# Kernel tuning notes

Hardware: AMD Instinct MI355X
Metric: run time of the kernel (lower is better)

Reference implementation:

```python
import jax, jax.numpy as jnp
import numpy as np

EMBED_DIM = 1024
B, C, H, W = 32, 1024, 32, 32


def _conv1x1(x, w, b):
    # x: [B,C,H,W], w: [O,C] (squeezed 1x1 conv kernel), b: [O]
    return jnp.einsum('bchw,oc->bohw', x, w) + b[None, :, None, None]


def setup_inputs() -> dict:
    key = jax.random.key(0)
    ks = jax.random.split(key, 12)
    s = 1.0 / np.sqrt(C)  # torch Conv2d default init scale (uniform bound)
    inp = {
        'shape_map': jax.random.normal(ks[0], (B, C, H, W), jnp.float32),
        'img_map': jax.random.normal(ks[1], (B, C, H, W), jnp.float32),
        'wq': jax.random.uniform(ks[2], (C, C), jnp.float32, -s, s),
        'bq': jax.random.uniform(ks[3], (C,), jnp.float32, -s, s),
        'wk': jax.random.uniform(ks[4], (C, C), jnp.float32, -s, s),
        'bk': jax.random.uniform(ks[5], (C,), jnp.float32, -s, s),
        'wv': jax.random.uniform(ks[6], (C, C), jnp.float32, -s, s),
        'bv': jax.random.uniform(ks[7], (C,), jnp.float32, -s, s),
        'wc': jax.random.uniform(ks[8], (C, C), jnp.float32, -s, s),
        'bc': jax.random.uniform(ks[9], (C,), jnp.float32, -s, s),
    }
    return inp


def reference(shape_map, img_map, wq, bq, wk, bk, wv, bv, wc, bc):
    # QKV embeddings: 1x1 conv + tanh (dropout is identity at inference)
    q = jnp.tanh(_conv1x1(shape_map, wq, bq))  # [B,C,H,W]
    k = jnp.tanh(_conv1x1(img_map, wk, bk))
    v = jnp.tanh(_conv1x1(img_map, wv, bv))

    hw = H * W
    q_flat = q.reshape(B, C, hw)
    k_flat = k.reshape(B, C, hw)
    v_flat = v.reshape(B, C, hw)

    # channel-attention: scores over channel pairs, contracted over spatial HW
    scores = jnp.einsum('bcs,bds->bcd', q_flat, k_flat) / jnp.sqrt(
        jnp.asarray(C, q_flat.dtype))  # [B,C,C]
    weights = jax.nn.softmax(scores, axis=-1)
    new_v = jnp.einsum('bcd,bds->bcs', weights, v_flat).reshape(B, C, H, W)

    out = _conv1x1(new_v, wc, bc) + shape_map
    return out
```

## Files before the change

### kernel.cpp

```cpp
#include <hip/hip_runtime.h>


typedef __bf16 bf16x8 __attribute__((ext_vector_type(8)));
typedef float floatx4 __attribute__((ext_vector_type(4)));

__device__ __forceinline__ unsigned short f2bf(float f) {
  union { float f; unsigned int u; } c; c.f = f;
  unsigned int u = c.u;
  u += 0x7fffu + ((u >> 16) & 1u);
  return (unsigned short)(u >> 16);
}

__device__ __forceinline__ float tanh_fast(float x) {
  x = fminf(15.0f, fmaxf(-15.0f, x));
  float t = __expf(2.0f * x);
  return (t - 1.0f) / (t + 1.0f);
}

__device__ __forceinline__ void gemm_core(
    const unsigned short* __restrict__ Ab,
    const unsigned short* __restrict__ Bb,
    int m0, int n0,
    unsigned short* lA, unsigned short* lB,
    floatx4 acc[4][4])
{
  constexpr int K = 1024;
  const int tid  = threadIdx.x;
  const int w    = tid >> 6;
  const int lane = tid & 63;
  const int quad = lane >> 4;
  const int lm   = lane & 15;
  const int wm   = (w >> 1) * 64;
  const int wn   = (w & 1) * 64;
  const int xr   = lm & 7;

  const int srow = lane >> 3;
  const int sg   = (lane & 7) ^ srow;
  const unsigned short* gA0 = Ab + (size_t)(m0 + srow) * K + sg * 8;
  const unsigned short* gB0 = Bb + (size_t)(n0 + srow) * K + sg * 8;

  for (int k0 = 0; k0 < K; k0 += 64) {
#pragma unroll
    for (int i = 0; i < 4; ++i) {
      const int q = w * 4 + i;
      __builtin_amdgcn_global_load_lds(
          (__attribute__((address_space(1))) void*)(gA0 + (size_t)q * 8 * K + k0),
          (__attribute__((address_space(3))) void*)(lA + q * 512), 16, 0, 0);
      __builtin_amdgcn_global_load_lds(
          (__attribute__((address_space(1))) void*)(gB0 + (size_t)q * 8 * K + k0),
          (__attribute__((address_space(3))) void*)(lB + q * 512), 16, 0, 0);
    }
    __syncthreads();

#pragma unroll
    for (int ks = 0; ks < 2; ++ks) {
      bf16x8 af[4], bfv[4];
#pragma unroll
      for (int i = 0; i < 4; ++i) {
        const int row = wm + 16 * i + lm;
        af[i] = *(const bf16x8*)(lA + row * 64 + (((ks * 4 + quad) ^ xr) * 8));
      }
#pragma unroll
      for (int j = 0; j < 4; ++j) {
        const int row = wn + 16 * j + lm;
        bfv[j] = *(const bf16x8*)(lB + row * 64 + (((ks * 4 + quad) ^ xr) * 8));
      }
#pragma unroll
      for (int i = 0; i < 4; ++i)
#pragma unroll
        for (int j = 0; j < 4; ++j)
          acc[i][j] = __builtin_amdgcn_mfma_f32_16x16x32_bf16(
              af[i], bfv[j], acc[i][j], 0, 0, 0);
    }
    __syncthreads();
  }
}

template<int OUT_F32, int BIAS_MODE , int TANH_ON, int RESID_ON>
__global__ __launch_bounds__(256, 2)
void gemm_bt(const unsigned short* __restrict__ A,
             const unsigned short* __restrict__ B,
             void* __restrict__ Cv,
             const float* __restrict__ bias,
             const float* __restrict__ resid,
             float scale,
             size_t sA, size_t sB, size_t sC, size_t sR)
{
  __shared__ unsigned short lA[128 * 64];
  __shared__ unsigned short lB[128 * 64];
  const int m0 = blockIdx.y * 128, n0 = blockIdx.x * 128;
  const int lane = threadIdx.x & 63, w = threadIdx.x >> 6;
  const int quad = lane >> 4, lm = lane & 15;
  const int wm = (w >> 1) * 64, wn = (w & 1) * 64;

  floatx4 acc[4][4];
#pragma unroll
  for (int i = 0; i < 4; ++i)
#pragma unroll
    for (int j = 0; j < 4; ++j) acc[i][j] = (floatx4)(0.0f);

  gemm_core(A + blockIdx.z * sA, B + blockIdx.z * sB, m0, n0, lA, lB, acc);

  float* Cf = (float*)Cv + blockIdx.z * sC;
  unsigned short* Cb = (unsigned short*)Cv + blockIdx.z * sC;
  const float* rp = RESID_ON ? (resid + blockIdx.z * sR) : (const float*)0;

#pragma unroll
  for (int i = 0; i < 4; ++i) {
    const int mbase = m0 + wm + 16 * i + quad * 4;
#pragma unroll
    for (int j = 0; j < 4; ++j) {
      const int n = n0 + wn + 16 * j + lm;
#pragma unroll
      for (int r = 0; r < 4; ++r) {
        const int m = mbase + r;
        float val = acc[i][j][r] * scale;
        if (BIAS_MODE == 1) val += bias[m];
        if (BIAS_MODE == 2) val += bias[n];
        if (TANH_ON) val = tanh_fast(val);
        if (RESID_ON) val += rp[(size_t)m * 1024 + n];
        if (OUT_F32) Cf[(size_t)m * 1024 + n] = val;
        else         Cb[(size_t)m * 1024 + n] = f2bf(val);
      }
    }
  }
}

__global__ __launch_bounds__(256, 2)
void qkv_gemm(const unsigned short* __restrict__ wqb,
              const unsigned short* __restrict__ wkb,
              const unsigned short* __restrict__ wvb,
              const unsigned short* __restrict__ Xt,
              const unsigned short* __restrict__ Yt,
              unsigned short* __restrict__ Qb,
              unsigned short* __restrict__ Kb,
              unsigned short* __restrict__ Vt,
              const float* __restrict__ bq,
              const float* __restrict__ bk,
              const float* __restrict__ bv,
              size_t sBf, int nb)
{
  __shared__ unsigned short lA[128 * 64];
  __shared__ unsigned short lB[128 * 64];
  const int z = blockIdx.z;
  int op, b;
  if (z >= 2 * nb)      { op = 2; b = z - 2 * nb; }
  else if (z >= nb)     { op = 1; b = z - nb; }
  else                  { op = 0; b = z; }

  const unsigned short *A, *B;
  unsigned short* C;
  const float* bias;
  int biasM;
  if (op == 0)      { A = wqb;            B = Xt + b * sBf; C = Qb + b * sBf; bias = bq; biasM = 1; }
  else if (op == 1) { A = wkb;            B = Yt + b * sBf; C = Kb + b * sBf; bias = bk; biasM = 1; }
  else              { A = Yt + b * sBf;   B = wvb;          C = Vt + b * sBf; bias = bv; biasM = 0; }

  const int m0 = blockIdx.y * 128, n0 = blockIdx.x * 128;
  const int lane = threadIdx.x & 63, w = threadIdx.x >> 6;
  const int quad = lane >> 4, lm = lane & 15;
  const int wm = (w >> 1) * 64, wn = (w & 1) * 64;

  floatx4 acc[4][4];
#pragma unroll
  for (int i = 0; i < 4; ++i)
#pragma unroll
    for (int j = 0; j < 4; ++j) acc[i][j] = (floatx4)(0.0f);

  gemm_core(A, B, m0, n0, lA, lB, acc);

#pragma unroll
  for (int i = 0; i < 4; ++i) {
    const int mbase = m0 + wm + 16 * i + quad * 4;
#pragma unroll
    for (int j = 0; j < 4; ++j) {
      const int n = n0 + wn + 16 * j + lm;
      const float bn = biasM ? 0.0f : bias[n];
#pragma unroll
      for (int r = 0; r < 4; ++r) {
        const int m = mbase + r;
        float val = acc[i][j][r] + (biasM ? bias[m] : bn);
        val = tanh_fast(val);
        C[(size_t)m * 1024 + n] = f2bf(val);
      }
    }
  }
}

__global__ __launch_bounds__(256)
void transpose2(const float* __restrict__ in0, const float* __restrict__ in1,
                unsigned short* __restrict__ out0, unsigned short* __restrict__ out1,
                size_t sIn, size_t sOut, int nb)
{
  __shared__ float tile[32][33];
  const int z = blockIdx.z;
  const float* in;
  unsigned short* out;
  if (z < nb) { in = in0 + (size_t)z * sIn;        out = out0 + (size_t)z * sOut; }
  else        { in = in1 + (size_t)(z - nb) * sIn; out = out1 + (size_t)(z - nb) * sOut; }

  const int x  = blockIdx.x * 32 + threadIdx.x;
  const int y0 = blockIdx.y * 32;
#pragma unroll
  for (int k = 0; k < 32; k += 8)
    tile[threadIdx.y + k][threadIdx.x] =
        in[(size_t)(y0 + threadIdx.y + k) * 1024 + x];
  __syncthreads();
  const int xo  = blockIdx.y * 32 + threadIdx.x;
  const int yo0 = blockIdx.x * 32;
#pragma unroll
  for (int k = 0; k < 32; k += 8)
    out[(size_t)(yo0 + threadIdx.y + k) * 1024 + xo] =
        f2bf(tile[threadIdx.x][threadIdx.y + k]);
}

__global__ __launch_bounds__(256)
void softmax_rows(const float* __restrict__ S, unsigned short* __restrict__ W,
                  size_t sS, size_t sW)
{
  const float* s = S + blockIdx.y * sS + (size_t)blockIdx.x * 1024;
  unsigned short* w = W + blockIdx.y * sW + (size_t)blockIdx.x * 1024;
  const int t = threadIdx.x;
  float4 v = ((const float4*)s)[t];
  float mx = fmaxf(fmaxf(v.x, v.y), fmaxf(v.z, v.w));
#pragma unroll
  for (int off = 32; off > 0; off >>= 1)
    mx = fmaxf(mx, __shfl_xor(mx, off));
  __shared__ float redm[4], reds[4];
  const int lane = t & 63, wv = t >> 6;
  if (lane == 0) redm[wv] = mx;
  __syncthreads();
  mx = fmaxf(fmaxf(redm[0], redm[1]), fmaxf(redm[2], redm[3]));
  float e0 = __expf(v.x - mx), e1 = __expf(v.y - mx),
        e2 = __expf(v.z - mx), e3 = __expf(v.w - mx);
  float sum = e0 + e1 + e2 + e3;
#pragma unroll
  for (int off = 32; off > 0; off >>= 1)
    sum += __shfl_xor(sum, off);
  if (lane == 0) reds[wv] = sum;
  __syncthreads();
  sum = reds[0] + reds[1] + reds[2] + reds[3];
  const float inv = 1.0f / sum;
  w[4 * t + 0] = f2bf(e0 * inv);
  w[4 * t + 1] = f2bf(e1 * inv);
  w[4 * t + 2] = f2bf(e2 * inv);
  w[4 * t + 3] = f2bf(e3 * inv);
}

__global__ __launch_bounds__(256)
void cvt_all(const float* __restrict__ s0, const float* __restrict__ s1,
             const float* __restrict__ s2, const float* __restrict__ s3,
             unsigned short* __restrict__ d0, unsigned short* __restrict__ d1,
             unsigned short* __restrict__ d2, unsigned short* __restrict__ d3)
{
  const float* in; unsigned short* out;
  switch (blockIdx.y) {
    case 0: in = s0; out = d0; break;
    case 1: in = s1; out = d1; break;
    case 2: in = s2; out = d2; break;
    default: in = s3; out = d3; break;
  }
  const int i = blockIdx.x * 256 + threadIdx.x;
  float4 v = ((const float4*)in)[i];
  ushort4 o;
  o.x = f2bf(v.x); o.y = f2bf(v.y); o.z = f2bf(v.z); o.w = f2bf(v.w);
  ((ushort4*)out)[i] = o;
}

extern "C" void kernel_launch(void* const* d_in, const int* in_sizes, int n_in,
                              void* d_out, int out_size, void* d_ws, size_t ws_size,
                              hipStream_t stream)
{
  const float* shape_map = (const float*)d_in[0];
  const float* img_map   = (const float*)d_in[1];
  const float* wq = (const float*)d_in[2];
  const float* bq = (const float*)d_in[3];
  const float* wk = (const float*)d_in[4];
  const float* bk = (const float*)d_in[5];
  const float* wv = (const float*)d_in[6];
  const float* bv = (const float*)d_in[7];
  const float* wc = (const float*)d_in[8];
  const float* bc = (const float*)d_in[9];
  float* out = (float*)d_out;

  const size_t ELT = 1024 * 1024;
  const size_t MB  = 1024 * 1024;
  char* ws = (char*)d_ws;

  unsigned short* wq_b = (unsigned short*)(ws + 0 * 2 * MB);
  unsigned short* wk_b = (unsigned short*)(ws + 1 * 2 * MB);
  unsigned short* wv_b = (unsigned short*)(ws + 2 * 2 * MB);
  unsigned short* wc_b = (unsigned short*)(ws + 3 * 2 * MB);
  char* slots = ws + 8 * MB;
  const size_t slotBytes = 10 * MB;
  int nslots = (ws_size > 8 * MB + slotBytes)
                   ? (int)((ws_size - 8 * MB) / slotBytes) : 1;
  if (nslots > 32) nslots = 32;
  if (nslots < 1)  nslots = 1;

  cvt_all<<<dim3(1024, 4), 256, 0, stream>>>(wq, wk, wv, wc,
                                             wq_b, wk_b, wv_b, wc_b);

  const size_t sBf = slotBytes / 2;
  const size_t sF  = slotBytes / 4;

  for (int c0 = 0; c0 < 32; c0 += nslots) {
    const int nb = (32 - c0 < nslots) ? (32 - c0) : nslots;

    unsigned short* Xt  = (unsigned short*)(slots + 0);
    unsigned short* Yt  = (unsigned short*)(slots + 2 * MB);
    float*          Sm  = (float*)(slots + 0);
    unsigned short* Qb  = (unsigned short*)(slots + 4 * MB);
    unsigned short* Kb  = (unsigned short*)(slots + 6 * MB);
    unsigned short* Vt  = (unsigned short*)(slots + 8 * MB);
    unsigned short* Wsm = Qb;
    unsigned short* NVt = Kb;

    transpose2<<<dim3(32, 32, 2 * nb), dim3(32, 8), 0, stream>>>(
        shape_map + (size_t)c0 * ELT, img_map + (size_t)c0 * ELT,
        Xt, Yt, ELT, sBf, nb);

    qkv_gemm<<<dim3(8, 8, 3 * nb), 256, 0, stream>>>(
        wq_b, wk_b, wv_b, Xt, Yt, Qb, Kb, Vt, bq, bk, bv, sBf, nb);

    gemm_bt<1, 0, 0, 0><<<dim3(8, 8, nb), 256, 0, stream>>>(
        Qb, Kb, Sm, nullptr, nullptr, 0.03125f, sBf, sBf, sF, 0);

    softmax_rows<<<dim3(1024, nb), 256, 0, stream>>>(Sm, Wsm, sF, sBf);

    gemm_bt<0, 0, 0, 0><<<dim3(8, 8, nb), 256, 0, stream>>>(
        Vt, Wsm, NVt, nullptr, nullptr, 1.0f, sBf, sBf, sBf, 0);

    gemm_bt<1, 1, 0, 1><<<dim3(8, 8, nb), 256, 0, stream>>>(
        wc_b, NVt, out + (size_t)c0 * ELT, bc,
        shape_map + (size_t)c0 * ELT, 1.0f, 0, sBf, ELT, ELT);
  }
}
```

Measured before the change: 1.010 ms.

## Use 256x256 double-buffered GEMM tiles with interleaved prefetch and 8 waves

Replaces the 128x128 single-buffered GEMM core with a 256x256 tile run by 512 threads (8 waves, each 128x64). The LDS tiles are double-buffered, and the next K-slice's global-to-LDS loads are spread across four MFMA phases, with explicit vmcnt waits, barriers and s_setprio around the MFMA bursts. The aim is to overlap memory latency with matrix math and raise data reuse per LDS byte. The cost is 128KB of LDS per block and many more accumulator registers, which may limit occupancy. It also cuts the grid to 16 tiles per batch, which may hurt load balance on 256 CUs.

```diff
diff --git a/kernel.cpp b/kernel.cpp
--- a/kernel.cpp
+++ b/kernel.cpp
@@ -17,67 +17,177 @@
   return (t - 1.0f) / (t + 1.0f);
 }
 
-__device__ __forceinline__ void gemm_core(
+__device__ __forceinline__ void stage16(unsigned short* dst,
+                                        const unsigned short* src) {
+  __builtin_amdgcn_global_load_lds(
+      (__attribute__((address_space(1))) void*)src,
+      (__attribute__((address_space(3))) void*)dst, 16, 0, 0);
+}
+
+__device__ __forceinline__ void gemm256_core(
     const unsigned short* __restrict__ Ab,
     const unsigned short* __restrict__ Bb,
     int m0, int n0,
     unsigned short* lA, unsigned short* lB,
-    floatx4 acc[4][4])
-{
-  constexpr int K = 1024;
+    floatx4 acc[8][4])
+{
+  constexpr int K  = 1024;
+  constexpr int NT = 16;
   const int tid  = threadIdx.x;
   const int w    = tid >> 6;
   const int lane = tid & 63;
   const int quad = lane >> 4;
   const int lm   = lane & 15;
-  const int wm   = (w >> 1) * 64;
-  const int wn   = (w & 1) * 64;
+  const int wm   = (w >> 2) * 128;
+  const int wn   = (w & 3) * 64;
   const int xr   = lm & 7;
 
-  const int srow = lane >> 3;
-  const int sg   = (lane & 7) ^ srow;
-  const unsigned short* gA0 = Ab + (size_t)(m0 + srow) * K + sg * 8;
-  const unsigned short* gB0 = Bb + (size_t)(n0 + srow) * K + sg * 8;
-
-  for (int k0 = 0; k0 < K; k0 += 64) {
-#pragma unroll
-    for (int i = 0; i < 4; ++i) {
-      const int q = w * 4 + i;
-      __builtin_amdgcn_global_load_lds(
-          (__attribute__((address_space(1))) void*)(gA0 + (size_t)q * 8 * K + k0),
-          (__attribute__((address_space(3))) void*)(lA + q * 512), 16, 0, 0);
-      __builtin_amdgcn_global_load_lds(
-          (__attribute__((address_space(1))) void*)(gB0 + (size_t)q * 8 * K + k0),
-          (__attribute__((address_space(3))) void*)(lB + q * 512), 16, 0, 0);
-    }
-    __syncthreads();
-
-#pragma unroll
-    for (int ks = 0; ks < 2; ++ks) {
-      bf16x8 af[4], bfv[4];
-#pragma unroll
-      for (int i = 0; i < 4; ++i) {
-        const int row = wm + 16 * i + lm;
-        af[i] = *(const bf16x8*)(lA + row * 64 + (((ks * 4 + quad) ^ xr) * 8));
-      }
-#pragma unroll
-      for (int j = 0; j < 4; ++j) {
-        const int row = wn + 16 * j + lm;
-        bfv[j] = *(const bf16x8*)(lB + row * 64 + (((ks * 4 + quad) ^ xr) * 8));
-      }
-#pragma unroll
-      for (int i = 0; i < 4; ++i)
+  const int srow = tid >> 3;
+  const int scg  = (lane & 7) ^ ((lane >> 3) & 7);
+  const unsigned short* gA = Ab + (size_t)(m0 + srow) * K + scg * 8;
+  const unsigned short* gB = Bb + (size_t)(n0 + srow) * K + scg * 8;
+  unsigned short* const dA = lA + w * 512;
+  unsigned short* const dB = lB + w * 512;
+
+#pragma unroll
+  for (int u = 0; u < 4; ++u) stage16(dA + u * 4096, gA + (size_t)(u * 64) * K);
+#pragma unroll
+  for (int u = 0; u < 4; ++u) stage16(dB + u * 4096, gB + (size_t)(u * 64) * K);
+  asm volatile("s_waitcnt vmcnt(0)" ::: "memory");
+  __builtin_amdgcn_s_barrier();
+
+  for (int kt = 0; kt < NT; ++kt) {
+    const int cb  = (kt & 1) * 16384;
+    const int nxb = 16384 - cb;
+    const unsigned short* cA = lA + cb;
+    const unsigned short* cB = lB + cb;
+    const int k1 = (kt + 1) << 6;
+    const bool st = (kt + 1) < NT;
+
+    bf16x8 bfr[4][2];
+
+    {
+      bf16x8 afr[2][2];
+#pragma unroll
+      for (int j = 0; j < 4; ++j)
+#pragma unroll
+        for (int kf = 0; kf < 2; ++kf)
+          bfr[j][kf] = *(const bf16x8*)(cB + (wn + 16 * j + lm) * 64 +
+                                        (((kf * 4 + quad) ^ xr) * 8));
+#pragma unroll
+      for (int i2 = 0; i2 < 2; ++i2)
+#pragma unroll
+        for (int kf = 0; kf < 2; ++kf)
+          afr[i2][kf] = *(const bf16x8*)(cA + (wm + 16 * i2 + lm) * 64 +
+                                         (((kf * 4 + quad) ^ xr) * 8));
+      if (st) {
+        stage16(dB + nxb + 0 * 4096, gB + (size_t)(0 * 64) * K + k1);
+        stage16(dB + nxb + 1 * 4096, gB + (size_t)(1 * 64) * K + k1);
+      }
+      __builtin_amdgcn_s_barrier();
+      asm volatile("s_waitcnt lgkmcnt(0)" ::: "memory");
+      __builtin_amdgcn_s_setprio(1);
+#pragma unroll
+      for (int i2 = 0; i2 < 2; ++i2)
 #pragma unroll
         for (int j = 0; j < 4; ++j)
-          acc[i][j] = __builtin_amdgcn_mfma_f32_16x16x32_bf16(
-              af[i], bfv[j], acc[i][j], 0, 0, 0);
-    }
-    __syncthreads();
+#pragma unroll
+          for (int kf = 0; kf < 2; ++kf)
+            acc[i2][j] = __builtin_amdgcn_mfma_f32_16x16x32_bf16(
+                afr[i2][kf], bfr[j][kf], acc[i2][j], 0, 0, 0);
+      __builtin_amdgcn_s_setprio(0);
+      __builtin_amdgcn_s_barrier();
+    }
+
+    {
+      bf16x8 afr[2][2];
+#pragma unroll
+      for (int i2 = 0; i2 < 2; ++i2)
+#pragma unroll
+        for (int kf = 0; kf < 2; ++kf)
+          afr[i2][kf] = *(const bf16x8*)(cA + (wm + 32 + 16 * i2 + lm) * 64 +
+                                         (((kf * 4 + quad) ^ xr) * 8));
+      if (st) {
+        stage16(dB + nxb + 2 * 4096, gB + (size_t)(2 * 64) * K + k1);
+        stage16(dB + nxb + 3 * 4096, gB + (size_t)(3 * 64) * K + k1);
+      }
+      __builtin_amdgcn_s_barrier();
+      asm volatile("s_waitcnt lgkmcnt(0)" ::: "memory");
+      __builtin_amdgcn_s_setprio(1);
+#pragma unroll
+      for (int i2 = 0; i2 < 2; ++i2)
+#pragma unroll
+        for (int j = 0; j < 4; ++j)
+#pragma unroll
+          for (int kf = 0; kf < 2; ++kf)
+            acc[2 + i2][j] = __builtin_amdgcn_mfma_f32_16x16x32_bf16(
+                afr[i2][kf], bfr[j][kf], acc[2 + i2][j], 0, 0, 0);
+      __builtin_amdgcn_s_setprio(0);
+      if (st) asm volatile("s_waitcnt vmcnt(4)" ::: "memory");
+      else    asm volatile("s_waitcnt vmcnt(0)" ::: "memory");
+      __builtin_amdgcn_s_barrier();
+    }
+
+    {
+      bf16x8 afr[2][2];
+#pragma unroll
+      for (int i2 = 0; i2 < 2; ++i2)
+#pragma unroll
+        for (int kf = 0; kf < 2; ++kf)
+          afr[i2][kf] = *(const bf16x8*)(cA + (wm + 64 + 16 * i2 + lm) * 64 +
+                                         (((kf * 4 + quad) ^ xr) * 8));
+      if (st) {
+        stage16(dA + nxb + 0 * 4096, gA + (size_t)(0 * 64) * K + k1);
+        stage16(dA + nxb + 2 * 4096, gA + (size_t)(2 * 64) * K + k1);
+      }
+      __builtin_amdgcn_s_barrier();
+      asm volatile("s_waitcnt lgkmcnt(0)" ::: "memory");
+      __builtin_amdgcn_s_setprio(1);
+#pragma unroll
+      for (int i2 = 0; i2 < 2; ++i2)
+#pragma unroll
+        for (int j = 0; j < 4; ++j)
+#pragma unroll
+          for (int kf = 0; kf < 2; ++kf)
+            acc[4 + i2][j] = __builtin_amdgcn_mfma_f32_16x16x32_bf16(
+                afr[i2][kf], bfr[j][kf], acc[4 + i2][j], 0, 0, 0);
+      __builtin_amdgcn_s_setprio(0);
+      __builtin_amdgcn_s_barrier();
+    }
+
+    {
+      bf16x8 afr[2][2];
+#pragma unroll
+      for (int i2 = 0; i2 < 2; ++i2)
+#pragma unroll
+        for (int kf = 0; kf < 2; ++kf)
+          afr[i2][kf] = *(const bf16x8*)(cA + (wm + 96 + 16 * i2 + lm) * 64 +
+                                         (((kf * 4 + quad) ^ xr) * 8));
+      if (st) {
+        stage16(dA + nxb + 1 * 4096, gA + (size_t)(1 * 64) * K + k1);
+        stage16(dA + nxb + 3 * 4096, gA + (size_t)(3 * 64) * K + k1);
+      }
+      __builtin_amdgcn_s_barrier();
+      asm volatile("s_waitcnt lgkmcnt(0)" ::: "memory");
+      __builtin_amdgcn_s_setprio(1);
+#pragma unroll
+      for (int i2 = 0; i2 < 2; ++i2)
+#pragma unroll
+        for (int j = 0; j < 4; ++j)
+#pragma unroll
+          for (int kf = 0; kf < 2; ++kf)
+            acc[6 + i2][j] = __builtin_amdgcn_mfma_f32_16x16x32_bf16(
+                afr[i2][kf], bfr[j][kf], acc[6 + i2][j], 0, 0, 0);
+      __builtin_amdgcn_s_setprio(0);
+      if (st) asm volatile("s_waitcnt vmcnt(2)" ::: "memory");
+      else    asm volatile("s_waitcnt vmcnt(0)" ::: "memory");
+      __builtin_amdgcn_s_barrier();
+    }
   }
 }
 
 template<int OUT_F32, int BIAS_MODE , int TANH_ON, int RESID_ON>
-__global__ __launch_bounds__(256, 2)
+__global__ __launch_bounds__(512, 2)
 void gemm_bt(const unsigned short* __restrict__ A,
              const unsigned short* __restrict__ B,
              void* __restrict__ Cv,
@@ -86,27 +196,27 @@
              float scale,
              size_t sA, size_t sB, size_t sC, size_t sR)
 {
-  __shared__ unsigned short lA[128 * 64];
-  __shared__ unsigned short lB[128 * 64];
-  const int m0 = blockIdx.y * 128, n0 = blockIdx.x * 128;
+  __shared__ unsigned short lA[2 * 16384];
+  __shared__ unsigned short lB[2 * 16384];
+  const int m0 = blockIdx.y * 256, n0 = blockIdx.x * 256;
   const int lane = threadIdx.x & 63, w = threadIdx.x >> 6;
   const int quad = lane >> 4, lm = lane & 15;
-  const int wm = (w >> 1) * 64, wn = (w & 1) * 64;
-
-  floatx4 acc[4][4];
-#pragma unroll
-  for (int i = 0; i < 4; ++i)
+  const int wm = (w >> 2) * 128, wn = (w & 3) * 64;
+
+  floatx4 acc[8][4];
+#pragma unroll
+  for (int i = 0; i < 8; ++i)
 #pragma unroll
     for (int j = 0; j < 4; ++j) acc[i][j] = (floatx4)(0.0f);
 
-  gemm_core(A + blockIdx.z * sA, B + blockIdx.z * sB, m0, n0, lA, lB, acc);
+  gemm256_core(A + blockIdx.z * sA, B + blockIdx.z * sB, m0, n0, lA, lB, acc);
 
   float* Cf = (float*)Cv + blockIdx.z * sC;
   unsigned short* Cb = (unsigned short*)Cv + blockIdx.z * sC;
   const float* rp = RESID_ON ? (resid + blockIdx.z * sR) : (const float*)0;
 
 #pragma unroll
-  for (int i = 0; i < 4; ++i) {
+  for (int i = 0; i < 8; ++i) {
     const int mbase = m0 + wm + 16 * i + quad * 4;
 #pragma unroll
     for (int j = 0; j < 4; ++j) {
@@ -126,7 +236,7 @@
   }
 }
 
-__global__ __launch_bounds__(256, 2)
+__global__ __launch_bounds__(512, 2)
 void qkv_gemm(const unsigned short* __restrict__ wqb,
               const unsigned short* __restrict__ wkb,
               const unsigned short* __restrict__ wvb,
@@ -140,8 +250,8 @@
               const float* __restrict__ bv,
               size_t sBf, int nb)
 {
-  __shared__ unsigned short lA[128 * 64];
-  __shared__ unsigned short lB[128 * 64];
+  __shared__ unsigned short lA[2 * 16384];
+  __shared__ unsigned short lB[2 * 16384];
   const int z = blockIdx.z;
   int op, b;
   if (z >= 2 * nb)      { op = 2; b = z - 2 * nb; }
@@ -156,21 +266,21 @@
   else if (op == 1) { A = wkb;            B = Yt + b * sBf; C = Kb + b * sBf; bias = bk; biasM = 1; }
   else              { A = Yt + b * sBf;   B = wvb;          C = Vt + b * sBf; bias = bv; biasM = 0; }
 
-  const int m0 = blockIdx.y * 128, n0 = blockIdx.x * 128;
+  const int m0 = blockIdx.y * 256, n0 = blockIdx.x * 256;
   const int lane = threadIdx.x & 63, w = threadIdx.x >> 6;
   const int quad = lane >> 4, lm = lane & 15;
-  const int wm = (w >> 1) * 64, wn = (w & 1) * 64;
-
-  floatx4 acc[4][4];
-#pragma unroll
-  for (int i = 0; i < 4; ++i)
+  const int wm = (w >> 2) * 128, wn = (w & 3) * 64;
+
+  floatx4 acc[8][4];
+#pragma unroll
+  for (int i = 0; i < 8; ++i)
 #pragma unroll
     for (int j = 0; j < 4; ++j) acc[i][j] = (floatx4)(0.0f);
 
-  gemm_core(A, B, m0, n0, lA, lB, acc);
-
-#pragma unroll
-  for (int i = 0; i < 4; ++i) {
+  gemm256_core(A, B, m0, n0, lA, lB, acc);
+
+#pragma unroll
+  for (int i = 0; i < 8; ++i) {
     const int mbase = m0 + wm + 16 * i + quad * 4;
 #pragma unroll
     for (int j = 0; j < 4; ++j) {
@@ -320,18 +430,18 @@
         shape_map + (size_t)c0 * ELT, img_map + (size_t)c0 * ELT,
         Xt, Yt, ELT, sBf, nb);
 
-    qkv_gemm<<<dim3(8, 8, 3 * nb), 256, 0, stream>>>(
+    qkv_gemm<<<dim3(4, 4, 3 * nb), 512, 0, stream>>>(
         wq_b, wk_b, wv_b, Xt, Yt, Qb, Kb, Vt, bq, bk, bv, sBf, nb);
 
-    gemm_bt<1, 0, 0, 0><<<dim3(8, 8, nb), 256, 0, stream>>>(
+    gemm_bt<1, 0, 0, 0><<<dim3(4, 4, nb), 512, 0, stream>>>(
         Qb, Kb, Sm, nullptr, nullptr, 0.03125f, sBf, sBf, sF, 0);
 
     softmax_rows<<<dim3(1024, nb), 256, 0, stream>>>(Sm, Wsm, sF, sBf);
 
-    gemm_bt<0, 0, 0, 0><<<dim3(8, 8, nb), 256, 0, stream>>>(
+    gemm_bt<0, 0, 0, 0><<<dim3(4, 4, nb), 512, 0, stream>>>(
         Vt, Wsm, NVt, nullptr, nullptr, 1.0f, sBf, sBf, sBf, 0);
 
-    gemm_bt<1, 1, 0, 1><<<dim3(8, 8, nb), 256, 0, stream>>>(
+    gemm_bt<1, 1, 0, 1><<<dim3(4, 4, nb), 512, 0, stream>>>(
         wc_b, NVt, out + (size_t)c0 * ELT, bc,
         shape_map + (size_t)c0 * ELT, 1.0f, 0, sBf, ELT, ELT);
   }
```

After: 995.9 us. No clear change (-1.4%).

## Double-buffer LDS tiles with K=32 steps to overlap loads with MFMA

Applied to the files above, without the earlier changes.

Replaces the single-buffered K=64 LDS staging loop with a double-buffered K=32 pipeline. Each iteration prefetches the next tile with global_load_lds while MFMAs run on the current tile, using explicit waitcnt, barriers and s_setprio around the MFMA block. Occupancy hint is raised from 2 to 3 blocks per SM, and the LDS swizzle is changed to fit 32-wide rows. In exchange there are twice as many barriers per K, and the higher occupancy target may constrain registers.

```diff
diff --git a/kernel.cpp b/kernel.cpp
--- a/kernel.cpp
+++ b/kernel.cpp
@@ -17,14 +17,22 @@
   return (t - 1.0f) / (t + 1.0f);
 }
 
-__device__ __forceinline__ void gemm_core(
+__device__ __forceinline__ void stage16(unsigned short* dst,
+                                        const unsigned short* src) {
+  __builtin_amdgcn_global_load_lds(
+      (__attribute__((address_space(1))) void*)src,
+      (__attribute__((address_space(3))) void*)dst, 16, 0, 0);
+}
+
+__device__ __forceinline__ void gemm128_core(
     const unsigned short* __restrict__ Ab,
     const unsigned short* __restrict__ Bb,
     int m0, int n0,
     unsigned short* lA, unsigned short* lB,
     floatx4 acc[4][4])
 {
-  constexpr int K = 1024;
+  constexpr int K  = 1024;
+  constexpr int NT = 32;
   const int tid  = threadIdx.x;
   const int w    = tid >> 6;
   const int lane = tid & 63;
@@ -32,52 +40,63 @@
   const int lm   = lane & 15;
   const int wm   = (w >> 1) * 64;
   const int wn   = (w & 1) * 64;
-  const int xr   = lm & 7;
-
-  const int srow = lane >> 3;
-  const int sg   = (lane & 7) ^ srow;
-  const unsigned short* gA0 = Ab + (size_t)(m0 + srow) * K + sg * 8;
-  const unsigned short* gB0 = Bb + (size_t)(n0 + srow) * K + sg * 8;
-
-  for (int k0 = 0; k0 < K; k0 += 64) {
-#pragma unroll
-    for (int i = 0; i < 4; ++i) {
-      const int q = w * 4 + i;
-      __builtin_amdgcn_global_load_lds(
-          (__attribute__((address_space(1))) void*)(gA0 + (size_t)q * 8 * K + k0),
-          (__attribute__((address_space(3))) void*)(lA + q * 512), 16, 0, 0);
-      __builtin_amdgcn_global_load_lds(
-          (__attribute__((address_space(1))) void*)(gB0 + (size_t)q * 8 * K + k0),
-          (__attribute__((address_space(3))) void*)(lB + q * 512), 16, 0, 0);
+  const int xr   = (lm >> 1) & 3;
+
+  const int srow = tid >> 2;
+  const int scg  = (tid & 3) ^ ((tid >> 3) & 3);
+  const unsigned short* gA = Ab + (size_t)(m0 + srow) * K + scg * 8;
+  const unsigned short* gB = Bb + (size_t)(n0 + srow) * K + scg * 8;
+  const int wbase = w * 512;
+
+  stage16(lA + wbase,        gA);
+  stage16(lA + 2048 + wbase, gA + (size_t)64 * K);
+  stage16(lB + wbase,        gB);
+  stage16(lB + 2048 + wbase, gB + (size_t)64 * K);
+  asm volatile("s_waitcnt vmcnt(0)" ::: "memory");
+  __builtin_amdgcn_s_barrier();
+
+  for (int kt = 0; kt < NT; ++kt) {
+    const int cur = (kt & 1) * 4096;
+    const int nx  = 4096 - cur;
+    const unsigned short* cA = lA + cur;
+    const unsigned short* cB = lB + cur;
+    const int k1 = (kt + 1) << 5;
+    const bool st = (kt + 1) < NT;
+
+    if (st) {
+      stage16(lA + nx + wbase,        gA + k1);
+      stage16(lA + nx + 2048 + wbase, gA + (size_t)64 * K + k1);
+      stage16(lB + nx + wbase,        gB + k1);
+      stage16(lB + nx + 2048 + wbase, gB + (size_t)64 * K + k1);
     }
-    __syncthreads();
-
-#pragma unroll
-    for (int ks = 0; ks < 2; ++ks) {
-      bf16x8 af[4], bfv[4];
-#pragma unroll
-      for (int i = 0; i < 4; ++i) {
-        const int row = wm + 16 * i + lm;
-        af[i] = *(const bf16x8*)(lA + row * 64 + (((ks * 4 + quad) ^ xr) * 8));
-      }
-#pragma unroll
-      for (int j = 0; j < 4; ++j) {
-        const int row = wn + 16 * j + lm;
-        bfv[j] = *(const bf16x8*)(lB + row * 64 + (((ks * 4 + quad) ^ xr) * 8));
-      }
-#pragma unroll
-      for (int i = 0; i < 4; ++i)
-#pragma unroll
-        for (int j = 0; j < 4; ++j)
-          acc[i][j] = __builtin_amdgcn_mfma_f32_16x16x32_bf16(
-              af[i], bfv[j], acc[i][j], 0, 0, 0);
-    }
-    __syncthreads();
+
+    bf16x8 af[4], bfv[4];
+#pragma unroll
+    for (int i = 0; i < 4; ++i)
+      af[i] = *(const bf16x8*)(cA + (wm + 16 * i + lm) * 32 +
+                               ((quad ^ xr) * 8));
+#pragma unroll
+    for (int j = 0; j < 4; ++j)
+      bfv[j] = *(const bf16x8*)(cB + (wn + 16 * j + lm) * 32 +
+                                ((quad ^ xr) * 8));
+
+    __builtin_amdgcn_s_barrier();
+    asm volatile("s_waitcnt lgkmcnt(0)" ::: "memory");
+    __builtin_amdgcn_s_setprio(1);
+#pragma unroll
+    for (int i = 0; i < 4; ++i)
+#pragma unroll
+      for (int j = 0; j < 4; ++j)
+        acc[i][j] = __builtin_amdgcn_mfma_f32_16x16x32_bf16(
+            af[i], bfv[j], acc[i][j], 0, 0, 0);
+    __builtin_amdgcn_s_setprio(0);
+    if (st) asm volatile("s_waitcnt vmcnt(0)" ::: "memory");
+    __builtin_amdgcn_s_barrier();
   }
 }
 
 template<int OUT_F32, int BIAS_MODE , int TANH_ON, int RESID_ON>
-__global__ __launch_bounds__(256, 2)
+__global__ __launch_bounds__(256, 3)
 void gemm_bt(const unsigned short* __restrict__ A,
              const unsigned short* __restrict__ B,
              void* __restrict__ Cv,
@@ -86,8 +105,8 @@
              float scale,
              size_t sA, size_t sB, size_t sC, size_t sR)
 {
-  __shared__ unsigned short lA[128 * 64];
-  __shared__ unsigned short lB[128 * 64];
+  __shared__ unsigned short lA[2 * 4096];
+  __shared__ unsigned short lB[2 * 4096];
   const int m0 = blockIdx.y * 128, n0 = blockIdx.x * 128;
   const int lane = threadIdx.x & 63, w = threadIdx.x >> 6;
   const int quad = lane >> 4, lm = lane & 15;
@@ -99,7 +118,7 @@
 #pragma unroll
     for (int j = 0; j < 4; ++j) acc[i][j] = (floatx4)(0.0f);
 
-  gemm_core(A + blockIdx.z * sA, B + blockIdx.z * sB, m0, n0, lA, lB, acc);
+  gemm128_core(A + blockIdx.z * sA, B + blockIdx.z * sB, m0, n0, lA, lB, acc);
 
   float* Cf = (float*)Cv + blockIdx.z * sC;
   unsigned short* Cb = (unsigned short*)Cv + blockIdx.z * sC;
@@ -126,7 +145,7 @@
   }
 }
 
-__global__ __launch_bounds__(256, 2)
+__global__ __launch_bounds__(256, 3)
 void qkv_gemm(const unsigned short* __restrict__ wqb,
               const unsigned short* __restrict__ wkb,
               const unsigned short* __restrict__ wvb,
@@ -140,8 +159,8 @@
               const float* __restrict__ bv,
               size_t sBf, int nb)
 {
-  __shared__ unsigned short lA[128 * 64];
-  __shared__ unsigned short lB[128 * 64];
+  __shared__ unsigned short lA[2 * 4096];
+  __shared__ unsigned short lB[2 * 4096];
   const int z = blockIdx.z;
   int op, b;
   if (z >= 2 * nb)      { op = 2; b = z - 2 * nb; }
@@ -167,7 +186,7 @@
 #pragma unroll
     for (int j = 0; j < 4; ++j) acc[i][j] = (floatx4)(0.0f);
 
-  gemm_core(A, B, m0, n0, lA, lB, acc);
+  gemm128_core(A, B, m0, n0, lA, lB, acc);
 
 #pragma unroll
   for (int i = 0; i < 4; ++i) {
```

Result: slower. 1.049 ms (+3.8%).
